# Kernel optimization log

Hardware: AMD Instinct MI355X
Metric: run time of the kernel (lower is better)

The kernel has to match this reference:

```python
import jax, jax.numpy as jnp
import numpy as np

N = 20000   # nodes
E = 320000  # edges
D_IN = 256
D_OUT = 256


def setup_inputs() -> dict:
    key = jax.random.key(0)
    ks = jax.random.split(key, 12)
    s = 0.05
    return {
        "h": jax.random.normal(ks[0], (N, D_OUT), jnp.float32),
        "x": jax.random.normal(ks[1], (N, D_IN), jnp.float32),
        "pos": jax.random.normal(ks[2], (N, 3), jnp.float32),
        "W_fc": jax.random.normal(ks[3], (D_OUT, D_IN + D_OUT), jnp.float32) * s,
        "b_fc": jax.random.normal(ks[4], (D_OUT,), jnp.float32) * s,
        "W_conv": jax.random.normal(ks[5], (D_OUT, D_OUT), jnp.float32) * s,
        "W_ih": jax.random.normal(ks[6], (3 * D_OUT, D_OUT), jnp.float32) * s,
        "W_hh": jax.random.normal(ks[7], (3 * D_OUT, D_OUT), jnp.float32) * s,
        "b_ih": jax.random.normal(ks[8], (3 * D_OUT,), jnp.float32) * s,
        "b_hh": jax.random.normal(ks[9], (3 * D_OUT,), jnp.float32) * s,
        "edge_index_gate": jax.random.randint(ks[10], (2, E), 0, N, jnp.int64),
        "edge_index_cand": jax.random.randint(ks[11], (2, E), 0, N, jnp.int64),
    }


def reference(h, x, pos, W_fc, b_fc, W_conv, W_ih, W_hh, b_ih, b_hh,
              edge_index_gate, edge_index_cand):
    # fc + relu on concatenated [x, h]
    xh = jnp.concatenate([x, h], axis=-1)            # [N, in+out]
    xr = jax.nn.relu(xh @ W_fc.T + b_fc)             # [N, out]

    # GatedGraphConv, num_layers=1, aggr='add'
    m = xr @ W_conv                                  # [N, out]  (x @ weight[0])
    src, dst = edge_index_gate[0], edge_index_gate[1]
    agg = jax.ops.segment_sum(m[src], dst, num_segments=xr.shape[0])  # [N, out]

    # GRUCell(agg, xr)  (torch semantics: input=agg, hidden=xr)
    gi = agg @ W_ih.T + b_ih                         # [N, 3*out]
    gh = xr @ W_hh.T + b_hh                          # [N, 3*out]
    i_r, i_z, i_n = jnp.split(gi, 3, axis=-1)
    h_r, h_z, h_n = jnp.split(gh, 3, axis=-1)
    r = jax.nn.sigmoid(i_r + h_r)
    z = jax.nn.sigmoid(i_z + h_z)
    n = jnp.tanh(i_n + r * h_n)
    h_next = (1.0 - z) * n + z * xr
    return h_next
```

## Files before the change

### kernel.cpp

```cpp
#include <hip/hip_runtime.h>
#include <hip/hip_bf16.h>

#define N_NODES 20000
#define MPAD 20032
#define CAP 64

typedef __attribute__((ext_vector_type(8))) short short8;
typedef __attribute__((ext_vector_type(4))) float f32x4;

#define MFMA16(a,b,c) __builtin_amdgcn_mfma_f32_16x16x32_bf16(a,b,c,0,0,0)

#define FSW(r) (((r) & 3) ^ (((r) >> 2) & 3))

#define WAIT_BAR(NSTR) do { \
  asm volatile("s_waitcnt vmcnt(" NSTR ") lgkmcnt(0)" ::: "memory"); \
  __builtin_amdgcn_s_barrier(); \
  __builtin_amdgcn_sched_barrier(0); \
} while (0)
#define END_BAR() do { \
  __builtin_amdgcn_sched_barrier(0); \
  __builtin_amdgcn_s_barrier(); \
} while (0)

static __device__ __forceinline__ ushort f2bf(float f) {
  union { float f; uint u; } v; v.f = f;
  uint u = v.u;
  uint r = (u + 0x7FFFu + ((u >> 16) & 1u)) >> 16;
  return (ushort)r;
}
static __device__ __forceinline__ float bf2f(ushort s) {
  union { uint u; float f; } v; v.u = ((uint)s) << 16; return v.f;
}

typedef __attribute__((address_space(1))) const unsigned int guint;
typedef __attribute__((address_space(3))) unsigned int luint;
static __device__ __forceinline__ void gl2lds16(const void* g, void* l) {
  __builtin_amdgcn_global_load_lds((guint*)g, (luint*)l, 16, 0, 0);
}

static __device__ __forceinline__ void cvt8(const float* __restrict__ s, ushort* __restrict__ d) {
  float4 v0 = *(const float4*)s;
  float4 v1 = *(const float4*)(s + 4);
  union { ushort u[8]; uint4 v; } t;
  t.u[0]=f2bf(v0.x); t.u[1]=f2bf(v0.y); t.u[2]=f2bf(v0.z); t.u[3]=f2bf(v0.w);
  t.u[4]=f2bf(v1.x); t.u[5]=f2bf(v1.y); t.u[6]=f2bf(v1.z); t.u[7]=f2bf(v1.w);
  *(uint4*)d = t.v;
}

__global__ __launch_bounds__(256) void k_prep(
    const float* __restrict__ Wfc, const float* __restrict__ Wc,
    const float* __restrict__ Wih, const float* __restrict__ Whh,
    ushort* __restrict__ WfcB, ushort* __restrict__ WcB,
    ushort* __restrict__ WihB, ushort* __restrict__ Bg3, int* __restrict__ cnt) {
  int i = blockIdx.x * 256 + threadIdx.x;
  if (i < 16384) cvt8(Wfc + i * 8, WfcB + i * 8);
  if (i < 8192)  cvt8(Wc  + i * 8, WcB  + i * 8);
  if (i < 24576) cvt8(Wih + i * 8, WihB + i * 8);
  if (i < 24576) {
    int row = i >> 5;
    int k0 = (i & 31) * 8;
    int g = row / 48, rem = row - g * 48;
    int p = rem >> 4, ci = rem & 15;
    int c = g * 16 + ci;
    cvt8(Whh + ((size_t)(p * 256 + c)) * 256 + k0, Bg3 + (size_t)row * 512 + 256 + k0);
  }
  if (i < N_NODES) cnt[i] = 0;
}

static __device__ __forceinline__ void fc_loadA(
    const float* __restrict__ x, const float* __restrict__ h,
    int gr, int gw, int ks, float4& v0, float4& v1) {
  const float* Af = (ks < 8) ? x : h;
  int ka = (ks * 32) & 255;
  const float* p = Af + (size_t)gr * 256 + ka + gw * 8;
  v0 = *(const float4*)p;
  v1 = *(const float4*)(p + 4);
}
static __device__ __forceinline__ void fc_writeA(ushort* sA, int r, int wl,
                                                 float4 v0, float4 v1) {
  union { ushort u[8]; uint4 v; } tmp;
  tmp.u[0]=f2bf(v0.x); tmp.u[1]=f2bf(v0.y); tmp.u[2]=f2bf(v0.z); tmp.u[3]=f2bf(v0.w);
  tmp.u[4]=f2bf(v1.x); tmp.u[5]=f2bf(v1.y); tmp.u[6]=f2bf(v1.z); tmp.u[7]=f2bf(v1.w);
  *(uint4*)&sA[r*32 + wl*8] = tmp.v;
}
static __device__ __forceinline__ void fc_stageB(
    const ushort* __restrict__ WfcB, ushort* sB, int col0, int t, int w, int ks) {
  int k0 = ks * 32;
  #pragma unroll
  for (int j = 0; j < 2; ++j) {
    int ci = j * 256 + t;
    int br = ci >> 2, wl = ci & 3;
    int gw = wl ^ FSW(br);
    gl2lds16(WfcB + (size_t)(col0 + br) * 512 + k0 + gw * 8,
             (char*)sB + (size_t)(j * 256 + w * 64) * 16);
  }
}

__global__ __launch_bounds__(256, 3) void k_mid(
    const float* __restrict__ x, const float* __restrict__ h,
    const ushort* __restrict__ WfcB, const float* __restrict__ bfc,
    ushort* __restrict__ AX,
    const ushort* __restrict__ WihB, const ushort* __restrict__ WcB,
    ushort* __restrict__ Bg3,
    const int* __restrict__ eg, int* __restrict__ cnt, int* __restrict__ srcs) {
  __shared__ __attribute__((aligned(16))) ushort smem[12288];
  int bid = blockIdx.x;
  int t = threadIdx.x, w = t >> 6, l = t & 63;

  if (bid >= 680) {
    int e = (bid - 680) * 256 + t;
    if (e < 320000) {
      int d = eg[320000 + e];
      int slot = atomicAdd(&cnt[d], 1);
      if (slot < CAP) srcs[d * CAP + slot] = eg[e];
    }
    return;
  }

  if (bid >= 632) {
    ushort* sA = smem;
    ushort* sB = smem + 2048;
    int wf = bid - 632;
    int row0 = (wf % 12) * 64, col0 = (wf / 12) * 64;
    int wr = (w >> 1) * 32, wc = (w & 1) * 32;
    f32x4 acc[2][2] = {};
    for (int ks = 0; ks < 8; ++ks) {
      int k0 = ks * 32;
      {
        int r = t >> 2, wl = t & 3;
        int gw = wl ^ FSW(r);
        gl2lds16(WihB + (size_t)(row0 + r) * 256 + k0 + gw * 8,
                 (char*)sA + (size_t)(w * 64) * 16);
      }
      {
        int r = t >> 2, wl = t & 3;
        int gw = wl ^ FSW(r);
        gl2lds16(WcB + (size_t)(col0 + r) * 256 + k0 + gw * 8,
                 (char*)sB + (size_t)(w * 64) * 16);
      }
      __syncthreads();
      short8 af[2], bfr[2];
      #pragma unroll
      for (int mi = 0; mi < 2; ++mi) {
        int r = wr + mi * 16 + (l & 15);
        af[mi] = *(short8*)&sA[r * 32 + (((l >> 4)) ^ FSW(r)) * 8];
      }
      #pragma unroll
      for (int ni = 0; ni < 2; ++ni) {
        int br = wc + ni * 16 + (l & 15);
        bfr[ni] = *(short8*)&sB[br * 32 + (((l >> 4)) ^ FSW(br)) * 8];
      }
      #pragma unroll
      for (int mi = 0; mi < 2; ++mi)
        #pragma unroll
        for (int ni = 0; ni < 2; ++ni)
          acc[mi][ni] = MFMA16(af[mi], bfr[ni], acc[mi][ni]);
      __syncthreads();
    }
    #pragma unroll
    for (int mi = 0; mi < 2; ++mi)
      #pragma unroll
      for (int ni = 0; ni < 2; ++ni)
        #pragma unroll
        for (int q = 0; q < 4; ++q) {
          int jj = row0 + wr + mi*16 + (l>>4)*4 + q;
          int tc = col0 + wc + ni*16 + (l&15);
          int p = jj >> 8, c = jj & 255;
          int brow = (c >> 4) * 48 + p * 16 + (c & 15);
          Bg3[(size_t)brow * 512 + tc] = f2bf(acc[mi][ni][q]);
        }
    return;
  }

  ushort* sA0 = smem;
  ushort* sA1 = smem + 2048;
  ushort* sB0 = smem + 4096;
  ushort* sB1 = smem + 8192;
  int wk = (bid & 7) * 79 + (bid >> 3);
  int panel = wk >> 1, ch = wk & 1;
  if (panel >= 313) return;
  int row0 = panel * 64, col0 = ch * 128;
  int wr = (w >> 1) * 32, wc = (w & 1) * 64;
  int r_ = t >> 2, wl_ = t & 3;
  int gw_ = wl_ ^ FSW(r_);
  int gr_ = row0 + r_; if (gr_ > N_NODES - 1) gr_ = N_NODES - 1;

  float4 va0, va1;
  fc_loadA(x, h, gr_, gw_, 0, va0, va1);
  fc_writeA(sA0, r_, wl_, va0, va1);
  fc_stageB(WfcB, sB0, col0, t, w, 0);
  fc_loadA(x, h, gr_, gw_, 1, va0, va1);
  __syncthreads();

  f32x4 acc[2][4] = {};
  #pragma unroll
  for (int ks = 0; ks < 16; ++ks) {
    ushort* cA = (ks & 1) ? sA1 : sA0;
    ushort* cB = (ks & 1) ? sB1 : sB0;
    ushort* nA = (ks & 1) ? sA0 : sA1;
    ushort* nB = (ks & 1) ? sB0 : sB1;
    if (ks < 15) {
      fc_writeA(nA, r_, wl_, va0, va1);
      fc_stageB(WfcB, nB, col0, t, w, ks + 1);
      if (ks < 14) fc_loadA(x, h, gr_, gw_, ks + 2, va0, va1);
    }
    if (ks < 13) WAIT_BAR("4");
    else         WAIT_BAR("0");
    short8 af[2], bfr[4];
    #pragma unroll
    for (int mi = 0; mi < 2; ++mi) {
      int r = wr + mi * 16 + (l & 15);
      af[mi] = *(short8*)&cA[r * 32 + (((l >> 4)) ^ FSW(r)) * 8];
    }
    #pragma unroll
    for (int ni = 0; ni < 4; ++ni) {
      int br = wc + ni * 16 + (l & 15);
      bfr[ni] = *(short8*)&cB[br * 32 + (((l >> 4)) ^ FSW(br)) * 8];
    }
    #pragma unroll
    for (int mi = 0; mi < 2; ++mi)
      #pragma unroll
      for (int ni = 0; ni < 4; ++ni)
        acc[mi][ni] = MFMA16(af[mi], bfr[ni], acc[mi][ni]);
    END_BAR();
  }
  #pragma unroll
  for (int mi = 0; mi < 2; ++mi)
    #pragma unroll
    for (int ni = 0; ni < 4; ++ni)
      #pragma unroll
      for (int q = 0; q < 4; ++q) {
        int r = row0 + wr + mi*16 + (l>>4)*4 + q;
        int c = col0 + wc + ni*16 + (l&15);
        if (r < N_NODES) {
          float v = acc[mi][ni][q] + bfc[c];
          v = v > 0.f ? v : 0.f;
          AX[(size_t)r * 512 + 256 + c] = f2bf(v);
        }
      }
}

__global__ __launch_bounds__(256) void k_aggS(
    const int* __restrict__ cnt, const int* __restrict__ srcs,
    ushort* __restrict__ AX) {
  int node = blockIdx.x * 8 + (threadIdx.x >> 5);
  if (node >= N_NODES) return;
  int lane = threadIdx.x & 31;
  const int* bkt = srcs + node * CAP;
  int n = cnt[node]; if (n > CAP) n = CAP;
  float a[8] = {};
  int i = 0;
  for (; i + 4 <= n; i += 4) {
    uint4 v0 = *(const uint4*)(AX + (size_t)bkt[i  ] * 512 + 256 + lane * 8);
    uint4 v1 = *(const uint4*)(AX + (size_t)bkt[i+1] * 512 + 256 + lane * 8);
    uint4 v2 = *(const uint4*)(AX + (size_t)bkt[i+2] * 512 + 256 + lane * 8);
    uint4 v3 = *(const uint4*)(AX + (size_t)bkt[i+3] * 512 + 256 + lane * 8);
    const ushort* p0 = (const ushort*)&v0; const ushort* p1 = (const ushort*)&v1;
    const ushort* p2 = (const ushort*)&v2; const ushort* p3 = (const ushort*)&v3;
    #pragma unroll
    for (int j = 0; j < 8; j++) a[j] += (bf2f(p0[j]) + bf2f(p1[j])) + (bf2f(p2[j]) + bf2f(p3[j]));
  }
  for (; i < n; ++i) {
    uint4 v0 = *(const uint4*)(AX + (size_t)bkt[i] * 512 + 256 + lane * 8);
    const ushort* p0 = (const ushort*)&v0;
    #pragma unroll
    for (int j = 0; j < 8; j++) a[j] += bf2f(p0[j]);
  }
  union { ushort s[8]; uint4 v; } o;
  #pragma unroll
  for (int j = 0; j < 8; j++) o.s[j] = f2bf(a[j]);
  *(uint4*)(AX + (size_t)node * 512 + lane * 8) = o.v;
}

static __device__ __forceinline__ void gru3_stage(
    const ushort* __restrict__ AX, const ushort* __restrict__ Bg3,
    ushort* sA, ushort* sB, int row0, int bro, int w, int l, int ks) {
  int k0 = ks * 64;
  #pragma unroll
  for (int j = 0; j < 2; ++j) {
    int rb = w * 16 + j * 8;
    int r = rb + (l >> 3);
    int gw = (l & 7) ^ (r & 7);
    gl2lds16(AX + (size_t)(row0 + r) * 512 + k0 + gw * 8, (char*)sA + (size_t)rb * 128);
  }
  #pragma unroll
  for (int j = 0; j < 6; ++j) {
    int rb = j * 32 + w * 8;
    int r = rb + (l >> 3);
    int gw = (l & 7) ^ (r & 7);
    gl2lds16(Bg3 + (size_t)(bro + r) * 512 + k0 + gw * 8, (char*)sB + (size_t)rb * 128);
  }
}

template<int PN>
static __device__ __forceinline__ void gru3_compute(
    const ushort* sA, const ushort* sB, int w, int l, f32x4 (&acc)[4][4]) {
  __builtin_amdgcn_s_setprio(1);
  #pragma unroll
  for (int j = 0; j < 2; ++j) {
    short8 af[4], bfr[3];
    #pragma unroll
    for (int mi = 0; mi < 4; ++mi) {
      int r = mi * 16 + (l & 15);
      af[mi] = *(const short8*)&sA[r * 64 + ((j * 4 + (l >> 4)) ^ (r & 7)) * 8];
    }
    #pragma unroll
    for (int p = 0; p < 3; ++p) {
      int br = w * 48 + p * 16 + (l & 15);
      bfr[p] = *(const short8*)&sB[br * 64 + ((j * 4 + (l >> 4)) ^ (br & 7)) * 8];
    }
    #pragma unroll
    for (int mi = 0; mi < 4; ++mi) {
      acc[mi][0]  = MFMA16(af[mi], bfr[0], acc[mi][0]);
      acc[mi][1]  = MFMA16(af[mi], bfr[1], acc[mi][1]);
      acc[mi][PN] = MFMA16(af[mi], bfr[2], acc[mi][PN]);
    }
  }
  __builtin_amdgcn_s_setprio(0);
}

__global__ __launch_bounds__(256, 2) void k_gru3(
    const ushort* __restrict__ AX, const ushort* __restrict__ Bg3,
    const float* __restrict__ bih, const float* __restrict__ bhh,
    float* __restrict__ out) {
  __shared__ __attribute__((aligned(16))) ushort smem[2 * 16384];
  ushort* sA0 = smem;
  ushort* sB0 = smem + 4096;
  ushort* sA1 = smem + 16384;
  ushort* sB1 = smem + 20480;
  int bid = blockIdx.x;
  int wk = (bid & 7) * 157 + (bid >> 3);
  int panel = wk >> 2, ch = wk & 3;
  if (panel >= 313) return;
  int row0 = panel * 64;
  int bro = ch * 192;
  int t = threadIdx.x, w = t >> 6, l = t & 63;

  gru3_stage(AX, Bg3, sA0, sB0, row0, bro, w, l, 0);
  __syncthreads();

  f32x4 acc[4][4] = {};
  #pragma unroll
  for (int ks = 0; ks < 8; ++ks) {
    ushort* cA = (ks & 1) ? sA1 : sA0;
    ushort* cB = (ks & 1) ? sB1 : sB0;
    ushort* nA = (ks & 1) ? sA0 : sA1;
    ushort* nB = (ks & 1) ? sB0 : sB1;
    if (ks < 7) gru3_stage(AX, Bg3, nA, nB, row0, bro, w, l, ks + 1);
    if (ks < 7) WAIT_BAR("8");
    else        WAIT_BAR("0");
    if (ks < 4) gru3_compute<2>(cA, cB, w, l, acc);
    else        gru3_compute<3>(cA, cB, w, l, acc);
    END_BAR();
  }

  int c = ch * 64 + w * 16 + (l & 15);
  float br_ = bih[c] + bhh[c];
  float bz_ = bih[256 + c] + bhh[256 + c];
  float bi_ = bih[512 + c];
  float bh_ = bhh[512 + c];
  #pragma unroll
  for (int mi = 0; mi < 4; ++mi)
    #pragma unroll
    for (int q = 0; q < 4; ++q) {
      int r = row0 + mi*16 + (l>>4)*4 + q;
      if (r < N_NODES) {
        float rg = 1.f / (1.f + __expf(-(acc[mi][0][q] + br_)));
        float zg = 1.f / (1.f + __expf(-(acc[mi][1][q] + bz_)));
        float ng = tanhf((acc[mi][2][q] + bi_) + rg * (acc[mi][3][q] + bh_));
        float xv = bf2f(AX[(size_t)r * 512 + 256 + c]);
        out[(size_t)r * 256 + c] = (1.f - zg) * ng + zg * xv;
      }
    }
}

extern "C" void kernel_launch(void* const* d_in, const int* in_sizes, int n_in,
                              void* d_out, int out_size, void* d_ws, size_t ws_size,
                              hipStream_t stream) {
  const float* h   = (const float*)d_in[0];
  const float* x   = (const float*)d_in[1];
  const float* Wfc = (const float*)d_in[3];
  const float* bfc = (const float*)d_in[4];
  const float* Wc  = (const float*)d_in[5];
  const float* Wih = (const float*)d_in[6];
  const float* Whh = (const float*)d_in[7];
  const float* bih = (const float*)d_in[8];
  const float* bhh = (const float*)d_in[9];
  const int*   eg  = (const int*)d_in[10];
  float* out = (float*)d_out;

  char* ws = (char*)d_ws;
  ushort* AX   = (ushort*)(ws);
  ushort* WfcB = (ushort*)(ws + 20512768);
  ushort* WcB  = (ushort*)(ws + 20774912);
  ushort* WihB = (ushort*)(ws + 20905984);
  ushort* Bg3  = (ushort*)(ws + 21299200);
  int*    cnt    = (int*)(ws + 22085632);
  int*    srcs   = (int*)(ws + 22165632);

  k_prep<<<512, 256, 0, stream>>>(Wfc, Wc, Wih, Whh, WfcB, WcB, WihB, Bg3, cnt);

  k_mid<<<1930, 256, 0, stream>>>(x, h, WfcB, bfc, AX, WihB, WcB, Bg3, eg, cnt, srcs);

  k_aggS<<<(N_NODES + 7) / 8, 256, 0, stream>>>(cnt, srcs, AX);

  k_gru3<<<1256, 256, 0, stream>>>(AX, Bg3, bih, bhh, out);
}
```

Baseline: 96.02 us.

## Pre-convert x/h to bf16 in prep and use triple-buffered async LDS staging in fc GEMM

The prep kernel now converts x and h into a concatenated bf16 buffer XH, so the fc GEMM can load A directly with global_load_lds instead of loading fp32 through registers and converting. The fc main loop moves to K-steps of 64 with a three-stage LDS ring buffer and an XOR swizzle, and occupancy is lowered to 2 blocks per CU to make room for the larger shared memory. This removes register-side conversion from the GEMM's critical path and deepens prefetch. The cost is an extra pass over x/h that writes and re-reads about 20 MB of bf16, and a much larger prep launch.

```diff
diff --git a/kernel.cpp b/kernel.cpp
--- a/kernel.cpp
+++ b/kernel.cpp
@@ -48,11 +48,17 @@
 }
 
 __global__ __launch_bounds__(256) void k_prep(
+    const float* __restrict__ x, const float* __restrict__ h,
     const float* __restrict__ Wfc, const float* __restrict__ Wc,
     const float* __restrict__ Wih, const float* __restrict__ Whh,
-    ushort* __restrict__ WfcB, ushort* __restrict__ WcB,
+    ushort* __restrict__ XH, ushort* __restrict__ WfcB, ushort* __restrict__ WcB,
     ushort* __restrict__ WihB, ushort* __restrict__ Bg3, int* __restrict__ cnt) {
   int i = blockIdx.x * 256 + threadIdx.x;
+  if (i < 1280000) {
+    int row = i >> 6, wi = i & 63;
+    if (wi < 32) cvt8(x + (size_t)row * 256 + wi * 8,        XH + (size_t)row * 512 + wi * 8);
+    else         cvt8(h + (size_t)row * 256 + (wi - 32) * 8, XH + (size_t)row * 512 + wi * 8);
+  }
   if (i < 16384) cvt8(Wfc + i * 8, WfcB + i * 8);
   if (i < 8192)  cvt8(Wc  + i * 8, WcB  + i * 8);
   if (i < 24576) cvt8(Wih + i * 8, WihB + i * 8);
@@ -67,43 +73,56 @@
   if (i < N_NODES) cnt[i] = 0;
 }
 
-static __device__ __forceinline__ void fc_loadA(
-    const float* __restrict__ x, const float* __restrict__ h,
-    int gr, int gw, int ks, float4& v0, float4& v1) {
-  const float* Af = (ks < 8) ? x : h;
-  int ka = (ks * 32) & 255;
-  const float* p = Af + (size_t)gr * 256 + ka + gw * 8;
-  v0 = *(const float4*)p;
-  v1 = *(const float4*)(p + 4);
-}
-static __device__ __forceinline__ void fc_writeA(ushort* sA, int r, int wl,
-                                                 float4 v0, float4 v1) {
-  union { ushort u[8]; uint4 v; } tmp;
-  tmp.u[0]=f2bf(v0.x); tmp.u[1]=f2bf(v0.y); tmp.u[2]=f2bf(v0.z); tmp.u[3]=f2bf(v0.w);
-  tmp.u[4]=f2bf(v1.x); tmp.u[5]=f2bf(v1.y); tmp.u[6]=f2bf(v1.z); tmp.u[7]=f2bf(v1.w);
-  *(uint4*)&sA[r*32 + wl*8] = tmp.v;
-}
-static __device__ __forceinline__ void fc_stageB(
-    const ushort* __restrict__ WfcB, ushort* sB, int col0, int t, int w, int ks) {
-  int k0 = ks * 32;
+static __device__ __forceinline__ void fc_stage(
+    const ushort* __restrict__ XH, const ushort* __restrict__ WfcB,
+    ushort* sA, ushort* sB, int row0, int col0, int w, int l, int ks) {
+  int k0 = ks * 64;
   #pragma unroll
   for (int j = 0; j < 2; ++j) {
-    int ci = j * 256 + t;
-    int br = ci >> 2, wl = ci & 3;
-    int gw = wl ^ FSW(br);
-    gl2lds16(WfcB + (size_t)(col0 + br) * 512 + k0 + gw * 8,
-             (char*)sB + (size_t)(j * 256 + w * 64) * 16);
-  }
-}
-
-__global__ __launch_bounds__(256, 3) void k_mid(
-    const float* __restrict__ x, const float* __restrict__ h,
-    const ushort* __restrict__ WfcB, const float* __restrict__ bfc,
-    ushort* __restrict__ AX,
+    int rb = w * 16 + j * 8;
+    int r = rb + (l >> 3);
+    int gw = (l & 7) ^ (r & 7);
+    gl2lds16(XH + (size_t)(row0 + r) * 512 + k0 + gw * 8, (char*)sA + (size_t)rb * 128);
+  }
+  #pragma unroll
+  for (int j = 0; j < 4; ++j) {
+    int rb = j * 32 + w * 8;
+    int r = rb + (l >> 3);
+    int gw = (l & 7) ^ (r & 7);
+    gl2lds16(WfcB + (size_t)(col0 + r) * 512 + k0 + gw * 8, (char*)sB + (size_t)rb * 128);
+  }
+}
+
+static __device__ __forceinline__ void fc_compute(
+    const ushort* sA, const ushort* sB, int wr, int wc, int l, f32x4 (&acc)[2][4]) {
+  #pragma unroll
+  for (int j = 0; j < 2; ++j) {
+    short8 af[2], bfr[4];
+    #pragma unroll
+    for (int mi = 0; mi < 2; ++mi) {
+      int r = wr + mi * 16 + (l & 15);
+      af[mi] = *(const short8*)&sA[r * 64 + ((j * 4 + (l >> 4)) ^ (r & 7)) * 8];
+    }
+    #pragma unroll
+    for (int ni = 0; ni < 4; ++ni) {
+      int br = wc + ni * 16 + (l & 15);
+      bfr[ni] = *(const short8*)&sB[br * 64 + ((j * 4 + (l >> 4)) ^ (br & 7)) * 8];
+    }
+    #pragma unroll
+    for (int mi = 0; mi < 2; ++mi)
+      #pragma unroll
+      for (int ni = 0; ni < 4; ++ni)
+        acc[mi][ni] = MFMA16(af[mi], bfr[ni], acc[mi][ni]);
+  }
+}
+
+__global__ __launch_bounds__(256, 2) void k_mid(
+    const ushort* __restrict__ XH, const ushort* __restrict__ WfcB,
+    const float* __restrict__ bfc, ushort* __restrict__ AX,
     const ushort* __restrict__ WihB, const ushort* __restrict__ WcB,
     ushort* __restrict__ Bg3,
     const int* __restrict__ eg, int* __restrict__ cnt, int* __restrict__ srcs) {
-  __shared__ __attribute__((aligned(16))) ushort smem[12288];
+  __shared__ __attribute__((aligned(16))) ushort smem[36864];
   int bid = blockIdx.x;
   int t = threadIdx.x, w = t >> 6, l = t & 63;
 
@@ -172,56 +191,33 @@
     return;
   }
 
-  ushort* sA0 = smem;
-  ushort* sA1 = smem + 2048;
-  ushort* sB0 = smem + 4096;
-  ushort* sB1 = smem + 8192;
+  ushort* A0 = smem;          ushort* B0 = smem + 4096;
+  ushort* A1 = smem + 12288;  ushort* B1 = smem + 16384;
+  ushort* A2 = smem + 24576;  ushort* B2 = smem + 28672;
   int wk = (bid & 7) * 79 + (bid >> 3);
   int panel = wk >> 1, ch = wk & 1;
   if (panel >= 313) return;
   int row0 = panel * 64, col0 = ch * 128;
   int wr = (w >> 1) * 32, wc = (w & 1) * 64;
-  int r_ = t >> 2, wl_ = t & 3;
-  int gw_ = wl_ ^ FSW(r_);
-  int gr_ = row0 + r_; if (gr_ > N_NODES - 1) gr_ = N_NODES - 1;
-
-  float4 va0, va1;
-  fc_loadA(x, h, gr_, gw_, 0, va0, va1);
-  fc_writeA(sA0, r_, wl_, va0, va1);
-  fc_stageB(WfcB, sB0, col0, t, w, 0);
-  fc_loadA(x, h, gr_, gw_, 1, va0, va1);
-  __syncthreads();
+
+  fc_stage(XH, WfcB, A0, B0, row0, col0, w, l, 0);
+  fc_stage(XH, WfcB, A1, B1, row0, col0, w, l, 1);
 
   f32x4 acc[2][4] = {};
   #pragma unroll
-  for (int ks = 0; ks < 16; ++ks) {
-    ushort* cA = (ks & 1) ? sA1 : sA0;
-    ushort* cB = (ks & 1) ? sB1 : sB0;
-    ushort* nA = (ks & 1) ? sA0 : sA1;
-    ushort* nB = (ks & 1) ? sB0 : sB1;
-    if (ks < 15) {
-      fc_writeA(nA, r_, wl_, va0, va1);
-      fc_stageB(WfcB, nB, col0, t, w, ks + 1);
-      if (ks < 14) fc_loadA(x, h, gr_, gw_, ks + 2, va0, va1);
-    }
-    if (ks < 13) WAIT_BAR("4");
-    else         WAIT_BAR("0");
-    short8 af[2], bfr[4];
-    #pragma unroll
-    for (int mi = 0; mi < 2; ++mi) {
-      int r = wr + mi * 16 + (l & 15);
-      af[mi] = *(short8*)&cA[r * 32 + (((l >> 4)) ^ FSW(r)) * 8];
-    }
-    #pragma unroll
-    for (int ni = 0; ni < 4; ++ni) {
-      int br = wc + ni * 16 + (l & 15);
-      bfr[ni] = *(short8*)&cB[br * 32 + (((l >> 4)) ^ FSW(br)) * 8];
-    }
-    #pragma unroll
-    for (int mi = 0; mi < 2; ++mi)
-      #pragma unroll
-      for (int ni = 0; ni < 4; ++ni)
-        acc[mi][ni] = MFMA16(af[mi], bfr[ni], acc[mi][ni]);
+  for (int ks = 0; ks < 8; ++ks) {
+    const int ci = ks % 3, ni2 = (ks + 2) % 3;
+    ushort* cA = (ci == 0) ? A0 : ((ci == 1) ? A1 : A2);
+    ushort* cB = (ci == 0) ? B0 : ((ci == 1) ? B1 : B2);
+    if (ks < 6) {
+      ushort* nA = (ni2 == 0) ? A0 : ((ni2 == 1) ? A1 : A2);
+      ushort* nB = (ni2 == 0) ? B0 : ((ni2 == 1) ? B1 : B2);
+      fc_stage(XH, WfcB, nA, nB, row0, col0, w, l, ks + 2);
+    }
+    if (ks < 6)      WAIT_BAR("12");
+    else if (ks == 6) WAIT_BAR("6");
+    else              WAIT_BAR("0");
+    fc_compute(cA, cB, wr, wc, l, acc);
     END_BAR();
   }
   #pragma unroll
@@ -391,16 +387,18 @@
 
   char* ws = (char*)d_ws;
   ushort* AX   = (ushort*)(ws);
-  ushort* WfcB = (ushort*)(ws + 20512768);
-  ushort* WcB  = (ushort*)(ws + 20774912);
-  ushort* WihB = (ushort*)(ws + 20905984);
-  ushort* Bg3  = (ushort*)(ws + 21299200);
-  int*    cnt    = (int*)(ws + 22085632);
-  int*    srcs   = (int*)(ws + 22165632);
-
-  k_prep<<<512, 256, 0, stream>>>(Wfc, Wc, Wih, Whh, WfcB, WcB, WihB, Bg3, cnt);
-
-  k_mid<<<1930, 256, 0, stream>>>(x, h, WfcB, bfc, AX, WihB, WcB, Bg3, eg, cnt, srcs);
+  ushort* XH   = (ushort*)(ws + 20512768);
+  ushort* WfcB = (ushort*)(ws + 41025536);
+  ushort* WcB  = (ushort*)(ws + 41287680);
+  ushort* WihB = (ushort*)(ws + 41418752);
+  ushort* Bg3  = (ushort*)(ws + 41811968);
+  int*    cnt    = (int*)(ws + 42598400);
+  int*    srcs   = (int*)(ws + 42678400);
+
+  k_prep<<<5000, 256, 0, stream>>>(x, h, Wfc, Wc, Wih, Whh,
+                                   XH, WfcB, WcB, WihB, Bg3, cnt);
+
+  k_mid<<<1930, 256, 0, stream>>>(XH, WfcB, bfc, AX, WihB, WcB, Bg3, eg, cnt, srcs);
 
   k_aggS<<<(N_NODES + 7) / 8, 256, 0, stream>>>(cnt, srcs, AX);
 
```

After: 102.7 us. +7.0%, slower.

## Shrink fc GEMM tile to 64x64 and drop double-buffered pipeline

Applied to the files above, without the earlier changes.

The fc+relu GEMM section of k_mid now uses 64x64 output tiles (four column chunks per row panel) instead of 64x128. It also replaces the double-buffered, software-pipelined LDS staging with a simple single-buffer load/sync/compute loop. This cuts shared memory and register use so occupancy can rise (launch bounds go to 4 blocks) and spreads the work over more blocks. In exchange, each x/h row is loaded and converted twice as often, and global load latency is no longer overlapped with MFMA work.

```diff
diff --git a/kernel.cpp b/kernel.cpp
--- a/kernel.cpp
+++ b/kernel.cpp
@@ -67,48 +67,19 @@
   if (i < N_NODES) cnt[i] = 0;
 }
 
-static __device__ __forceinline__ void fc_loadA(
-    const float* __restrict__ x, const float* __restrict__ h,
-    int gr, int gw, int ks, float4& v0, float4& v1) {
-  const float* Af = (ks < 8) ? x : h;
-  int ka = (ks * 32) & 255;
-  const float* p = Af + (size_t)gr * 256 + ka + gw * 8;
-  v0 = *(const float4*)p;
-  v1 = *(const float4*)(p + 4);
-}
-static __device__ __forceinline__ void fc_writeA(ushort* sA, int r, int wl,
-                                                 float4 v0, float4 v1) {
-  union { ushort u[8]; uint4 v; } tmp;
-  tmp.u[0]=f2bf(v0.x); tmp.u[1]=f2bf(v0.y); tmp.u[2]=f2bf(v0.z); tmp.u[3]=f2bf(v0.w);
-  tmp.u[4]=f2bf(v1.x); tmp.u[5]=f2bf(v1.y); tmp.u[6]=f2bf(v1.z); tmp.u[7]=f2bf(v1.w);
-  *(uint4*)&sA[r*32 + wl*8] = tmp.v;
-}
-static __device__ __forceinline__ void fc_stageB(
-    const ushort* __restrict__ WfcB, ushort* sB, int col0, int t, int w, int ks) {
-  int k0 = ks * 32;
-  #pragma unroll
-  for (int j = 0; j < 2; ++j) {
-    int ci = j * 256 + t;
-    int br = ci >> 2, wl = ci & 3;
-    int gw = wl ^ FSW(br);
-    gl2lds16(WfcB + (size_t)(col0 + br) * 512 + k0 + gw * 8,
-             (char*)sB + (size_t)(j * 256 + w * 64) * 16);
-  }
-}
-
-__global__ __launch_bounds__(256, 3) void k_mid(
+__global__ __launch_bounds__(256, 4) void k_mid(
     const float* __restrict__ x, const float* __restrict__ h,
     const ushort* __restrict__ WfcB, const float* __restrict__ bfc,
     ushort* __restrict__ AX,
     const ushort* __restrict__ WihB, const ushort* __restrict__ WcB,
     ushort* __restrict__ Bg3,
     const int* __restrict__ eg, int* __restrict__ cnt, int* __restrict__ srcs) {
-  __shared__ __attribute__((aligned(16))) ushort smem[12288];
+  __shared__ __attribute__((aligned(16))) ushort smem[4096];
   int bid = blockIdx.x;
   int t = threadIdx.x, w = t >> 6, l = t & 63;
 
-  if (bid >= 680) {
-    int e = (bid - 680) * 256 + t;
+  if (bid >= 1304) {
+    int e = (bid - 1304) * 256 + t;
     if (e < 320000) {
       int d = eg[320000 + e];
       int slot = atomicAdd(&cnt[d], 1);
@@ -117,10 +88,10 @@
     return;
   }
 
-  if (bid >= 632) {
+  if (bid >= 1256) {
     ushort* sA = smem;
     ushort* sB = smem + 2048;
-    int wf = bid - 632;
+    int wf = bid - 1256;
     int row0 = (wf % 12) * 64, col0 = (wf / 12) * 64;
     int wr = (w >> 1) * 32, wc = (w & 1) * 32;
     f32x4 acc[2][2] = {};
@@ -172,62 +143,56 @@
     return;
   }
 
-  ushort* sA0 = smem;
-  ushort* sA1 = smem + 2048;
-  ushort* sB0 = smem + 4096;
-  ushort* sB1 = smem + 8192;
-  int wk = (bid & 7) * 79 + (bid >> 3);
-  int panel = wk >> 1, ch = wk & 1;
+  ushort* sA = smem;
+  ushort* sB = smem + 2048;
+  int wk = (bid & 7) * 157 + (bid >> 3);
+  int panel = wk >> 2, ch = wk & 3;
   if (panel >= 313) return;
-  int row0 = panel * 64, col0 = ch * 128;
-  int wr = (w >> 1) * 32, wc = (w & 1) * 64;
+  int row0 = panel * 64, col0 = ch * 64;
+  int wr = (w >> 1) * 32, wc = (w & 1) * 32;
   int r_ = t >> 2, wl_ = t & 3;
   int gw_ = wl_ ^ FSW(r_);
   int gr_ = row0 + r_; if (gr_ > N_NODES - 1) gr_ = N_NODES - 1;
 
-  float4 va0, va1;
-  fc_loadA(x, h, gr_, gw_, 0, va0, va1);
-  fc_writeA(sA0, r_, wl_, va0, va1);
-  fc_stageB(WfcB, sB0, col0, t, w, 0);
-  fc_loadA(x, h, gr_, gw_, 1, va0, va1);
-  __syncthreads();
-
-  f32x4 acc[2][4] = {};
-  #pragma unroll
+  f32x4 acc[2][2] = {};
   for (int ks = 0; ks < 16; ++ks) {
-    ushort* cA = (ks & 1) ? sA1 : sA0;
-    ushort* cB = (ks & 1) ? sB1 : sB0;
-    ushort* nA = (ks & 1) ? sA0 : sA1;
-    ushort* nB = (ks & 1) ? sB0 : sB1;
-    if (ks < 15) {
-      fc_writeA(nA, r_, wl_, va0, va1);
-      fc_stageB(WfcB, nB, col0, t, w, ks + 1);
-      if (ks < 14) fc_loadA(x, h, gr_, gw_, ks + 2, va0, va1);
-    }
-    if (ks < 13) WAIT_BAR("4");
-    else         WAIT_BAR("0");
-    short8 af[2], bfr[4];
+    int k0 = ks * 32;
+    const float* Af = (ks < 8) ? x : h;
+    int ka = k0 & 255;
+    {
+      union { ushort u[8]; uint4 v; } tmp;
+      const float* p = Af + (size_t)gr_ * 256 + ka + gw_ * 8;
+      float4 v0 = *(const float4*)p;
+      float4 v1 = *(const float4*)(p + 4);
+      tmp.u[0]=f2bf(v0.x); tmp.u[1]=f2bf(v0.y); tmp.u[2]=f2bf(v0.z); tmp.u[3]=f2bf(v0.w);
+      tmp.u[4]=f2bf(v1.x); tmp.u[5]=f2bf(v1.y); tmp.u[6]=f2bf(v1.z); tmp.u[7]=f2bf(v1.w);
+      *(uint4*)&sA[r_*32 + wl_*8] = tmp.v;
+    }
+    gl2lds16(WfcB + (size_t)(col0 + r_) * 512 + k0 + gw_ * 8,
+             (char*)sB + (size_t)(w * 64) * 16);
+    __syncthreads();
+    short8 af[2], bfr[2];
     #pragma unroll
     for (int mi = 0; mi < 2; ++mi) {
       int r = wr + mi * 16 + (l & 15);
-      af[mi] = *(short8*)&cA[r * 32 + (((l >> 4)) ^ FSW(r)) * 8];
-    }
-    #pragma unroll
-    for (int ni = 0; ni < 4; ++ni) {
+      af[mi] = *(short8*)&sA[r * 32 + (((l >> 4)) ^ FSW(r)) * 8];
+    }
+    #pragma unroll
+    for (int ni = 0; ni < 2; ++ni) {
       int br = wc + ni * 16 + (l & 15);
-      bfr[ni] = *(short8*)&cB[br * 32 + (((l >> 4)) ^ FSW(br)) * 8];
+      bfr[ni] = *(short8*)&sB[br * 32 + (((l >> 4)) ^ FSW(br)) * 8];
     }
     #pragma unroll
     for (int mi = 0; mi < 2; ++mi)
       #pragma unroll
-      for (int ni = 0; ni < 4; ++ni)
+      for (int ni = 0; ni < 2; ++ni)
         acc[mi][ni] = MFMA16(af[mi], bfr[ni], acc[mi][ni]);
-    END_BAR();
+    __syncthreads();
   }
   #pragma unroll
   for (int mi = 0; mi < 2; ++mi)
     #pragma unroll
-    for (int ni = 0; ni < 4; ++ni)
+    for (int ni = 0; ni < 2; ++ni)
       #pragma unroll
       for (int q = 0; q < 4; ++q) {
         int r = row0 + wr + mi*16 + (l>>4)*4 + q;
@@ -400,7 +365,7 @@
 
   k_prep<<<512, 256, 0, stream>>>(Wfc, Wc, Wih, Whh, WfcB, WcB, WihB, Bg3, cnt);
 
-  k_mid<<<1930, 256, 0, stream>>>(x, h, WfcB, bfc, AX, WihB, WcB, Bg3, eg, cnt, srcs);
+  k_mid<<<2554, 256, 0, stream>>>(x, h, WfcB, bfc, AX, WihB, WcB, Bg3, eg, cnt, srcs);
 
   k_aggS<<<(N_NODES + 7) / 8, 256, 0, stream>>>(cnt, srcs, AX);
 
```

Result: no change. 95.85 us (-0.2%).
